# Kernel optimization log

Hardware: AMD Instinct MI355X
Metric: run time of the kernel (lower is better)

Reference implementation:

```python
import jax, jax.numpy as jnp
import numpy as np
from jax import lax

CONTEXT = 7
EPS = 1e-5  # BatchNorm2d default eps
DN = ('NCHW', 'OIHW', 'NCHW')


def _cbr(x, W, b, g, be, m, v, padding):
    # conv2d + BatchNorm (eval, running stats) + ReLU
    y = lax.conv_general_dilated(x, W, (1, 1), padding, dimension_numbers=DN)
    y = y + b[None, :, None, None]
    y = (y - m[None, :, None, None]) * (g / jnp.sqrt(v + EPS))[None, :, None, None] + be[None, :, None, None]
    return jax.nn.relu(y)


def _pool21(x):  # MaxPool2d(kernel_size=(2,1))
    return lax.reduce_window(x, -jnp.inf, lax.max, (1, 1, 2, 1), (1, 1, 2, 1), 'VALID')


def setup_inputs() -> dict:
    key = jax.random.key(0)
    ks = jax.random.split(key, 16)
    B, T, F, NC = 16, 108, 144, 25
    d = {}
    d['x'] = jax.random.normal(ks[0], (B, T, F), jnp.float32)
    d['labels'] = jax.random.randint(ks[1], (B, T), 0, NC)
    shapes = [(32, 1, 3, 3), (32, 32, 3, 3), (32, 32, 3, 3), (32, 32, 3, 3),
              (64, 32, 3, 3), (64, 64, 3, 3), (128, 64, 12, 9)]
    for i, s in enumerate(shapes, 1):
        fan_in = s[1] * s[2] * s[3]
        d[f'W{i}'] = jax.random.normal(ks[1 + i], s, jnp.float32) / np.sqrt(fan_in).astype(np.float32)
        c = s[0]
        d[f'b{i}'] = jnp.zeros((c,), jnp.float32)
        d[f'g{i}'] = jnp.ones((c,), jnp.float32)
        d[f'be{i}'] = jnp.zeros((c,), jnp.float32)
        d[f'm{i}'] = jnp.zeros((c,), jnp.float32)
        d[f'v{i}'] = jnp.ones((c,), jnp.float32)
    d['W8'] = jax.random.normal(ks[9], (NC, 128, 1, 1), jnp.float32) / np.float32(np.sqrt(128.0))
    d['b8'] = jnp.zeros((NC,), jnp.float32)
    return d


def reference(x, labels,
              W1, b1, g1, be1, m1, v1,
              W2, b2, g2, be2, m2, v2,
              W3, b3, g3, be3, m3, v3,
              W4, b4, g4, be4, m4, v4,
              W5, b5, g5, be5, m5, v5,
              W6, b6, g6, be6, m6, v6,
              W7, b7, g7, be7, m7, v7,
              W8, b8):
    B, T, F = x.shape
    win_len = 2 * CONTEXT + 1
    # permute to [B, F, T], zero-pad time by CONTEXT on both sides
    xp = jnp.pad(jnp.transpose(x, (0, 2, 1)), ((0, 0), (0, 0), (CONTEXT, CONTEXT)))
    # vectorized sliding windows (replaces the nested python loop of slices+cat)
    idx = jnp.arange(T)[:, None] + jnp.arange(win_len)[None, :]  # [T, 15]
    win = xp[:, :, idx]                                          # [B, F, T, 15]
    h = jnp.transpose(win, (0, 2, 1, 3)).reshape(B * T, 1, F, win_len)
    h = _cbr(h, W1, b1, g1, be1, m1, v1, 'SAME')
    h = _cbr(h, W2, b2, g2, be2, m2, v2, 'SAME')
    h = _cbr(h, W3, b3, g3, be3, m3, v3, 'SAME')
    h = _cbr(h, W4, b4, g4, be4, m4, v4, 'SAME')
    h = _pool21(h)  # dropout2d is identity in eval
    h = _cbr(h, W5, b5, g5, be5, m5, v5, 'VALID')
    h = _cbr(h, W6, b6, g6, be6, m6, v6, 'VALID')
    h = _pool21(h)
    h = _cbr(h, W7, b7, g7, be7, m7, v7, 'VALID')
    h = lax.conv_general_dilated(h, W8, (1, 1), 'VALID', dimension_numbers=DN) + b8[None, :, None, None]
    logits = jnp.mean(h, axis=(2, 3))  # AvgPool2d over full spatial extent
    return logits.reshape(B, T, -1)    # probs_out=True -> CRF input
```

## Files before the change

kernel.cpp:

```cpp
#include <hip/hip_runtime.h>
#include <hip/hip_bf16.h>
#include <hip/hip_fp16.h>

#define TA 71680
#define TB 69120
#define SLOT 140800
#define C6N 26112

typedef _Float16 v8h __attribute__((ext_vector_type(8)));
typedef float v4f __attribute__((ext_vector_type(4)));
typedef unsigned short u16x8 __attribute__((ext_vector_type(8)));

__device__ inline float h2f(unsigned short u) {
    union { unsigned short s; _Float16 h; } v; v.s = u; return (float)v.h;
}
__device__ inline unsigned short f2h(float f) {
    union { unsigned short s; _Float16 h; } v; v.h = (_Float16)f; return v.s;
}

__global__ void repack_k(const float* __restrict__ W, const float* __restrict__ bb,
                         const float* __restrict__ gg, const float* __restrict__ be,
                         const float* __restrict__ mm, const float* __restrict__ vv,
                         float* __restrict__ wOut, float* __restrict__ tOut,
                         int CIN, int KHW, int COUT)
{
    int gid = blockIdx.x * 256 + threadIdx.x;
    if (gid < COUT) {
        float s = gg[gid] * rsqrtf(vv[gid] + 1e-5f);
        tOut[gid] = (bb[gid] - mm[gid]) * s + be[gid];
    }
    int tot = CIN * KHW * COUT;
    if (gid >= tot) return;
    int co = gid % COUT;
    int rest = gid / COUT;
    int k = rest % KHW;
    int ci = rest / KHW;
    float s = gg[co] * rsqrtf(vv[co] + 1e-5f);
    wOut[gid] = W[(co * CIN + ci) * KHW + k] * s;
}

__global__ void repack_mfma_k(const float* __restrict__ W, const float* __restrict__ bb,
                              const float* __restrict__ gg, const float* __restrict__ be,
                              const float* __restrict__ mm, const float* __restrict__ vv,
                              unsigned short* __restrict__ frag, float* __restrict__ tOut,
                              int CIN, int NT, int HALVES)
{
    int gid = blockIdx.x * 256 + threadIdx.x;
    int COUT = NT * 16;
    if (gid < COUT) {
        float s = gg[gid] * rsqrtf(vv[gid] + 1e-5f);
        tOut[gid] = (bb[gid] - mm[gid]) * s + be[gid];
    }
    int tot = 9 * HALVES * NT * 512;
    if (gid >= tot) return;
    int j    = gid & 7;
    int lane = (gid >> 3) & 63;
    int nt   = (gid >> 9) % NT;
    int rest = (gid >> 9) / NT;
    int half = rest % HALVES;
    int khw  = rest / HALVES;
    int ci   = half * 32 + (lane >> 4) * 8 + j;
    int co   = nt * 16 + (lane & 15);
    int kh   = khw / 3, kw = khw % 3;
    float s = gg[co] * rsqrtf(vv[co] + 1e-5f);
    frag[gid] = f2h(W[((co * CIN + ci) * 3 + kh) * 3 + kw] * s);
}

__global__ void repack7_k(const float* __restrict__ W, const float* __restrict__ bb,
                          const float* __restrict__ gg, const float* __restrict__ be,
                          const float* __restrict__ mm, const float* __restrict__ vv,
                          unsigned short* __restrict__ frag, float* __restrict__ tOut)
{
    int gid = blockIdx.x * 256 + threadIdx.x;
    if (gid < 128) {
        float s = gg[gid] * rsqrtf(vv[gid] + 1e-5f);
        tOut[gid] = (bb[gid] - mm[gid]) * s + be[gid];
    }
    if (gid >= 884736) return;
    int j    = gid & 7;
    int lane = (gid >> 3) & 63;
    int nt   = (gid >> 9) & 7;
    int half = (gid >> 12) & 1;
    int khw  = gid >> 13;
    int co   = nt * 16 + (lane & 15);
    int ci   = half * 32 + (lane >> 4) * 8 + j;
    int kh   = khw / 9, kw = khw - kh * 9;
    float s = gg[co] * rsqrtf(vv[co] + 1e-5f);
    frag[gid] = f2h(W[((co * 64 + ci) * 12 + kh) * 9 + kw] * s);
}

__global__ __launch_bounds__(256) void conv1_k(
    const float* __restrict__ x, unsigned short* __restrict__ out,
    const float* __restrict__ wr, const float* __restrict__ tv,
    int c0, int cn)
{
    int gid = blockIdx.x * 256 + threadIdx.x;
    if (gid >= cn * 2160) return;
    int nl = gid / 2160, p = gid - nl * 2160;
    int f = p / 15, w = p - f * 15;
    int n = c0 + nl;
    int b = n / 108, t = n - b * 108;

    float acc[32];
#pragma unroll
    for (int i = 0; i < 32; ++i) acc[i] = 0.f;

    for (int kh = 0; kh < 3; ++kh) {
        int ff = f + kh - 1;
        if (ff < 0 || ff >= 144) continue;
        for (int kw = 0; kw < 3; ++kw) {
            int c = w + kw - 1;
            if (c < 0 || c >= 15) continue;
            int tt = t + c - 7;
            if (tt < 0 || tt >= 108) continue;
            float xval = x[(b * 108 + tt) * 144 + ff];
            const float* wp = wr + (kh * 3 + kw) * 32;
#pragma unroll
            for (int q = 0; q < 8; ++q) {
                float4 wv = *(const float4*)(wp + q * 4);
                acc[q * 4 + 0] = fmaf(xval, wv.x, acc[q * 4 + 0]);
                acc[q * 4 + 1] = fmaf(xval, wv.y, acc[q * 4 + 1]);
                acc[q * 4 + 2] = fmaf(xval, wv.z, acc[q * 4 + 2]);
                acc[q * 4 + 3] = fmaf(xval, wv.w, acc[q * 4 + 3]);
            }
        }
    }
    unsigned short* ob = out + (size_t)nl * SLOT + (f * 15 + w) * 8;
#pragma unroll
    for (int cg = 0; cg < 4; ++cg) {
        u16x8 pk;
#pragma unroll
        for (int c = 0; c < 8; ++c)
            pk[c] = f2h(fmaxf(acc[cg * 8 + c] + tv[cg * 8 + c], 0.f));
        *(u16x8*)(ob + cg * 17280) = pk;
    }
}

template<bool POOL>
__global__ __launch_bounds__(256) void conv234m_k(
    const unsigned short* __restrict__ in, unsigned short* __restrict__ out,
    const unsigned short* __restrict__ frag, const float* __restrict__ tv)
{
    __shared__ __align__(16) unsigned short sA[9824];
    const int band = blockIdx.x;
    const int n = blockIdx.y;
    const int tid = threadIdx.x;
    const int wave = tid >> 6, lane = tid & 63;
    const int m = lane & 15, quad = lane >> 4;

    {
        const float4* src = (const float4*)(in + (size_t)n * SLOT);
        float4* dst = (float4*)sA;
        for (int i = tid; i < 1224; i += 256) {
            int q = i / 306, pos = i - q * 306;
            int r = pos / 17, c = pos - r * 17;
            int ir = band * 16 + r - 1;
            int ic = c - 1;
            float4 v = {0.f, 0.f, 0.f, 0.f};
            if (ir >= 0 && ir < 144 && ic >= 0 && ic < 15)
                v = src[q * 2160 + ir * 15 + ic];
            dst[q * 307 + pos] = v;
        }
    }
    __syncthreads();

    int mt[4], la0[4];
#pragma unroll
    for (int wt = 0; wt < 4; ++wt) {
        int t = wave * 4 + wt; if (t > 14) t = 14;
        mt[wt] = t;
        int p = band * 240 + t * 16 + m;
        int r, w;
        if (POOL) { int pr = p / 30, rem = p - pr * 30; w = rem >> 1; r = pr * 2 + (rem & 1); }
        else      { r = p / 15; w = p - r * 15; }
        la0[wt] = ((r - band * 16) * 17 + w) * 8;
    }

    v4f acc[2][4];
#pragma unroll
    for (int nt = 0; nt < 2; ++nt)
#pragma unroll
        for (int wt = 0; wt < 4; ++wt) acc[nt][wt] = (v4f){0.f,0.f,0.f,0.f};

    const unsigned short* sQ = sA + quad * 307 * 8;
#pragma unroll
    for (int khw = 0; khw < 9; ++khw) {
        const int shift = ((khw / 3) * 17 + (khw % 3)) * 8;
        v8h a[4];
#pragma unroll
        for (int wt = 0; wt < 4; ++wt)
            a[wt] = *(const v8h*)(sQ + la0[wt] + shift);
#pragma unroll
        for (int nt = 0; nt < 2; ++nt) {
            v8h b = *(const v8h*)(frag + (khw * 2 + nt) * 512 + lane * 8);
#pragma unroll
            for (int wt = 0; wt < 4; ++wt)
                acc[nt][wt] = __builtin_amdgcn_mfma_f32_16x16x32_f16(a[wt], b, acc[nt][wt], 0, 0, 0);
        }
    }

    unsigned short* outN = out + (size_t)n * SLOT;
#pragma unroll
    for (int wt = 0; wt < 4; ++wt) {
        const int pb = band * 240 + mt[wt] * 16 + quad * 4;
#pragma unroll
        for (int nt = 0; nt < 2; ++nt) {
            const int co = nt * 16 + m;
            const float tb = tv[co];
            unsigned short* ob = outN + (co >> 3) * (POOL ? 9216 : 17280) + (co & 7);
            if (POOL) {
#pragma unroll
                for (int pi = 0; pi < 2; ++pi) {
                    int pe = pb + pi * 2;
                    int pr = pe / 30, rem = pe - pr * 30, w = rem >> 1;
                    float v0 = fmaxf(acc[nt][wt][pi * 2] + tb, 0.f);
                    float v1 = fmaxf(acc[nt][wt][pi * 2 + 1] + tb, 0.f);
                    ob[(pr * 16 + w) * 8] = f2h(fmaxf(v0, v1));
                }
            } else {
#pragma unroll
                for (int reg = 0; reg < 4; ++reg) {
                    int pr = pb + reg;
                    int f = pr / 15, w = pr - f * 15;
                    ob[(f * 15 + w) * 8] = f2h(fmaxf(acc[nt][wt][reg] + tb, 0.f));
                }
            }
        }
    }
}

__global__ __launch_bounds__(256) void conv5m_k(
    const unsigned short* __restrict__ in, unsigned short* __restrict__ out,
    const unsigned short* __restrict__ frag, const float* __restrict__ tv)
{
    const int n = blockIdx.y;
    const int tid = threadIdx.x;
    const int wave = tid >> 6, lane = tid & 63;
    const int m = lane & 15, quad = lane >> 4;
    const unsigned short* inN = in + (size_t)n * SLOT + quad * 9216;

    int mt[2], a0[2];
#pragma unroll
    for (int wt = 0; wt < 2; ++wt) {
        int t = blockIdx.x * 8 + wave * 2 + wt; if (t > 56) t = 56;
        mt[wt] = t;
        int p = t * 16 + m; if (p > 909) p = 909;
        int r = p / 13, w = p - r * 13;
        a0[wt] = (r * 16 + w) * 8;
    }

    v4f acc[4][2];
#pragma unroll
    for (int nt = 0; nt < 4; ++nt)
#pragma unroll
        for (int wt = 0; wt < 2; ++wt) acc[nt][wt] = (v4f){0.f,0.f,0.f,0.f};

#pragma unroll
    for (int khw = 0; khw < 9; ++khw) {
        const int shift = ((khw / 3) * 16 + (khw % 3)) * 8;
        v8h a[2];
#pragma unroll
        for (int wt = 0; wt < 2; ++wt)
            a[wt] = *(const v8h*)(inN + a0[wt] + shift);
#pragma unroll
        for (int nt = 0; nt < 4; ++nt) {
            v8h b = *(const v8h*)(frag + (khw * 4 + nt) * 512 + lane * 8);
#pragma unroll
            for (int wt = 0; wt < 2; ++wt)
                acc[nt][wt] = __builtin_amdgcn_mfma_f32_16x16x32_f16(a[wt], b, acc[nt][wt], 0, 0, 0);
        }
    }

    unsigned short* outN = out + (size_t)n * SLOT;
#pragma unroll
    for (int wt = 0; wt < 2; ++wt) {
        const int pb = mt[wt] * 16 + quad * 4;
#pragma unroll
        for (int nt = 0; nt < 4; ++nt) {
            const int co = nt * 16 + m;
            const float tb = tv[co];
            unsigned short* ob = outN + (co >> 3) * 8960 + (co & 7);
#pragma unroll
            for (int reg = 0; reg < 4; ++reg) {
                int p = pb + reg;
                if (p < 910) {
                    int r = p / 13, w = p - r * 13;
                    ob[(r * 16 + w) * 8] = f2h(fmaxf(acc[nt][wt][reg] + tb, 0.f));
                }
            }
        }
    }
}

__global__ __launch_bounds__(256) void conv6m_k(
    const unsigned short* __restrict__ in, unsigned short* __restrict__ c6,
    const unsigned short* __restrict__ frag, const float* __restrict__ tv)
{
    const int n = blockIdx.y;
    const int tid = threadIdx.x;
    const int wave = tid >> 6, lane = tid & 63;
    const int m = lane & 15, quad = lane >> 4;
    const unsigned short* inN = in + (size_t)n * SLOT;

    int mt[2], a0[2];
#pragma unroll
    for (int wt = 0; wt < 2; ++wt) {
        int t = blockIdx.x * 8 + wave * 2 + wt; if (t > 46) t = 46;
        mt[wt] = t;
        int p = t * 16 + m; if (p > 747) p = 747;
        int pr = p / 22, rem = p - pr * 22;
        int w = rem >> 1, r = pr * 2 + (rem & 1);
        a0[wt] = (r * 16 + w) * 8;
    }

    v4f acc[4][2];
#pragma unroll
    for (int nt = 0; nt < 4; ++nt)
#pragma unroll
        for (int wt = 0; wt < 2; ++wt) acc[nt][wt] = (v4f){0.f,0.f,0.f,0.f};

#pragma unroll
    for (int khw = 0; khw < 9; ++khw) {
        const int shift = ((khw / 3) * 16 + (khw % 3)) * 8;
#pragma unroll
        for (int half = 0; half < 2; ++half) {
            const unsigned short* ip = inN + (half * 4 + quad) * 8960 + shift;
            v8h a[2];
#pragma unroll
            for (int wt = 0; wt < 2; ++wt)
                a[wt] = *(const v8h*)(ip + a0[wt]);
#pragma unroll
            for (int nt = 0; nt < 4; ++nt) {
                v8h b = *(const v8h*)(frag + ((khw * 2 + half) * 4 + nt) * 512 + lane * 8);
#pragma unroll
                for (int wt = 0; wt < 2; ++wt)
                    acc[nt][wt] = __builtin_amdgcn_mfma_f32_16x16x32_f16(a[wt], b, acc[nt][wt], 0, 0, 0);
            }
        }
    }

    unsigned short* outN = c6 + (size_t)n * C6N;
#pragma unroll
    for (int wt = 0; wt < 2; ++wt) {
        const int pb = mt[wt] * 16 + quad * 4;
#pragma unroll
        for (int nt = 0; nt < 4; ++nt) {
            const int co = nt * 16 + m;
            const float tb = tv[co];
            unsigned short* ob = outN + (co >> 3) * 3264 + (co & 7);
#pragma unroll
            for (int pi = 0; pi < 2; ++pi) {
                int pe = pb + pi * 2;
                if (pe < 748) {
                    int pr = pe / 22, rem = pe - pr * 22, w = rem >> 1;
                    float v0 = fmaxf(acc[nt][wt][pi * 2] + tb, 0.f);
                    float v1 = fmaxf(acc[nt][wt][pi * 2 + 1] + tb, 0.f);
                    ob[(pr * 12 + w) * 8] = f2h(fmaxf(v0, v1));
                }
            }
        }
    }
}

__global__ __launch_bounds__(256) void conv7mfma_k(
    const unsigned short* __restrict__ c6, float* __restrict__ pooled,
    const unsigned short* __restrict__ frag7, const float* __restrict__ tv)
{
    __shared__ __align__(16) unsigned short sA[14176];
    const int n = blockIdx.x;
    const int tid = threadIdx.x;
    const int wave = tid >> 6;
    const int lane = tid & 63;
    const int m = lane & 15;
    const int quad = lane >> 4;

    int pm[5];
#pragma unroll
    for (int mt = 0; mt < 5; ++mt) {
        int p = mt * 16 + m;
        if (p >= 69) p = 0;
        pm[mt] = (p / 3) * 13 + (p % 3);
    }

    v4f acc[2][5];
#pragma unroll
    for (int t = 0; t < 2; ++t)
#pragma unroll
        for (int mt = 0; mt < 5; ++mt)
            acc[t][mt] = (v4f){0.f, 0.f, 0.f, 0.f};

    for (int half = 0; half < 2; ++half) {
        __syncthreads();
        {
            const float4* src = (const float4*)(c6 + (size_t)n * C6N + half * 13056);
            float4* dst = (float4*)sA;
            for (int i = tid; i < 1632; i += 256) {
                int q = i / 408, pos = i - q * 408;
                int h = pos / 12, w = pos - h * 12;
                dst[q * 443 + h * 13 + w] = src[i];
            }
        }
        __syncthreads();
        for (int khw = 0; khw < 108; ++khw) {
            const int off = (khw / 9) * 13 + (khw % 9);
            v8h a[5];
#pragma unroll
            for (int mt = 0; mt < 5; ++mt)
                a[mt] = *(const v8h*)(sA + (quad * 443 + pm[mt] + off) * 8);
            const unsigned short* bp = frag7
                + ((size_t)(khw * 2 + half) * 8) * 512 + lane * 8;
#pragma unroll
            for (int t = 0; t < 2; ++t) {
                const int nt = wave + t * 4;
                v8h b = *(const v8h*)(bp + nt * 512);
#pragma unroll
                for (int mt = 0; mt < 5; ++mt)
                    acc[t][mt] = __builtin_amdgcn_mfma_f32_16x16x32_f16(
                        a[mt], b, acc[t][mt], 0, 0, 0);
            }
        }
    }

    float s[2] = {0.f, 0.f};
#pragma unroll
    for (int t = 0; t < 2; ++t) {
        const float tb = tv[(wave + t * 4) * 16 + m];
#pragma unroll
        for (int mt = 0; mt < 5; ++mt) {
#pragma unroll
            for (int rr = 0; rr < 4; ++rr) {
                int p = mt * 16 + quad * 4 + rr;
                if (p < 69) s[t] += fmaxf(acc[t][mt][rr] + tb, 0.f);
            }
        }
    }
#pragma unroll
    for (int t = 0; t < 2; ++t) {
        s[t] += __shfl_xor(s[t], 16);
        s[t] += __shfl_xor(s[t], 32);
    }
    if (lane < 16) {
#pragma unroll
        for (int t = 0; t < 2; ++t)
            pooled[(size_t)n * 128 + (wave + t * 4) * 16 + lane] = s[t] * (1.f / 69.f);
    }
}

__global__ void logits_k(const float* __restrict__ pooled, const float* __restrict__ W8,
                         const float* __restrict__ b8, float* __restrict__ outg,
                         int total)
{
    int gid = blockIdx.x * 256 + threadIdx.x;
    if (gid >= total * 25) return;
    int nl = gid / 25, c = gid - nl * 25;
    const float* pp = pooled + (size_t)nl * 128;
    const float* wp = W8 + c * 128;
    float s = b8[c];
#pragma unroll
    for (int ci = 0; ci < 128; ci += 4) {
        float4 wv = *(const float4*)(wp + ci);
        float4 pv = *(const float4*)(pp + ci);
        s = fmaf(wv.x, pv.x, s);
        s = fmaf(wv.y, pv.y, s);
        s = fmaf(wv.z, pv.z, s);
        s = fmaf(wv.w, pv.w, s);
    }
    outg[(size_t)nl * 25 + c] = s;
}

extern "C" void kernel_launch(void* const* d_in, const int* in_sizes, int n_in,
                              void* d_out, int out_size, void* d_ws, size_t ws_size,
                              hipStream_t stream)
{
    const float* x = (const float*)d_in[0];
    const float* Wl[8]; const float* bl[8]; const float* gl[8];
    const float* bel[8]; const float* ml[8]; const float* vl[8];
    for (int i = 1; i <= 7; ++i) {
        int o = 2 + (i - 1) * 6;
        Wl[i]  = (const float*)d_in[o + 0];
        bl[i]  = (const float*)d_in[o + 1];
        gl[i]  = (const float*)d_in[o + 2];
        bel[i] = (const float*)d_in[o + 3];
        ml[i]  = (const float*)d_in[o + 4];
        vl[i]  = (const float*)d_in[o + 5];
    }
    const float* W8 = (const float*)d_in[44];
    const float* b8 = (const float*)d_in[45];
    float* ws = (float*)d_ws;

    float* wr1 = ws + 0;        float* t1 = ws + 288;
    unsigned short* f2b = (unsigned short*)(ws + 320);
    float* t2 = ws + 4928;
    unsigned short* f3b = (unsigned short*)(ws + 4960);
    float* t3 = ws + 9568;
    unsigned short* f4b = (unsigned short*)(ws + 9600);
    float* t4 = ws + 14208;
    unsigned short* f5b = (unsigned short*)(ws + 14240);
    float* t5 = ws + 23456;
    unsigned short* f6b = (unsigned short*)(ws + 23520);
    float* t6 = ws + 41952;
    unsigned short* f7b = (unsigned short*)(ws + 42016);
    float* t7 = ws + 484384;
    const size_t WFL = 484512;

    unsigned short* c6buf = (unsigned short*)(ws + WFL);
    const size_t C6FL = (size_t)1728 * C6N / 2;
    float* pooled = ws + WFL + C6FL;
    const size_t FIXED = WFL + C6FL + (size_t)1728 * 128;

    size_t avail_fl = ws_size / 4;
    size_t buf_halves = (avail_fl > FIXED) ? (avail_fl - FIXED) * 2 : 0;
    int Cs = (int)(buf_halves / (size_t)SLOT);
    if (Cs < 1) Cs = 1;
    if (Cs > 1728) Cs = 1728;
    unsigned short* bufA = (unsigned short*)(ws + FIXED);
    unsigned short* bufB = bufA + TA;

    auto g1 = [](int t) { return (t + 255) / 256; };

    repack_k<<<g1(288), 256, 0, stream>>>(Wl[1], bl[1], gl[1], bel[1], ml[1], vl[1], wr1, t1, 1, 9, 32);
    repack_mfma_k<<<g1(9216),  256, 0, stream>>>(Wl[2], bl[2], gl[2], bel[2], ml[2], vl[2], f2b, t2, 32, 2, 1);
    repack_mfma_k<<<g1(9216),  256, 0, stream>>>(Wl[3], bl[3], gl[3], bel[3], ml[3], vl[3], f3b, t3, 32, 2, 1);
    repack_mfma_k<<<g1(9216),  256, 0, stream>>>(Wl[4], bl[4], gl[4], bel[4], ml[4], vl[4], f4b, t4, 32, 2, 1);
    repack_mfma_k<<<g1(18432), 256, 0, stream>>>(Wl[5], bl[5], gl[5], bel[5], ml[5], vl[5], f5b, t5, 32, 4, 1);
    repack_mfma_k<<<g1(36864), 256, 0, stream>>>(Wl[6], bl[6], gl[6], bel[6], ml[6], vl[6], f6b, t6, 64, 4, 2);
    repack7_k<<<g1(884736), 256, 0, stream>>>(Wl[7], bl[7], gl[7], bel[7], ml[7], vl[7], f7b, t7);

    for (int c0 = 0; c0 < 1728; c0 += Cs) {
        int cn = (1728 - c0 < Cs) ? (1728 - c0) : Cs;
        conv1_k<<<g1(cn * 2160), 256, 0, stream>>>(x, bufA, wr1, t1, c0, cn);
        conv234m_k<false><<<dim3(9, cn), 256, 0, stream>>>(bufA, bufB, f2b, t2);
        conv234m_k<false><<<dim3(9, cn), 256, 0, stream>>>(bufB, bufA, f3b, t3);
        conv234m_k<true ><<<dim3(9, cn), 256, 0, stream>>>(bufA, bufB, f4b, t4);
        conv5m_k<<<dim3(8, cn), 256, 0, stream>>>(bufB, bufA, f5b, t5);
        conv6m_k<<<dim3(6, cn), 256, 0, stream>>>(bufA, c6buf + (size_t)c0 * C6N, f6b, t6);
    }

    conv7mfma_k<<<1728, 256, 0, stream>>>(c6buf, pooled, f7b, t7);
    logits_k<<<g1(1728 * 25), 256, 0, stream>>>(pooled, W8, b8, (float*)d_out, 1728);
}
```

Measured before the change: 1.170 ms.

## Fuse conv2/conv3/conv4 into one kernel with halo recompute in LDS

Replaces three separate conv234 launches with one kernel. Each block loads a 16-row band plus a 3-row halo, computes conv2 and conv3 over the enlarged tile in shared memory, then conv4 with fused pooling writes to global. This removes two global round trips of intermediate activations and two launches, at the cost of recomputing halo rows and using more LDS per block. It also compacts the c6 buffer layout (row stride 12 to 11) so conv7 can load with a plain linear copy, and shrinks SLOT/C6N.

New measurement: 1.134 ms. 1.03x faster.

```diff
diff --git a/kernel.cpp b/kernel.cpp
--- a/kernel.cpp
+++ b/kernel.cpp
@@ -3,9 +3,8 @@
 #include <hip/hip_fp16.h>
 
 #define TA 71680
-#define TB 69120
-#define SLOT 140800
-#define C6N 26112
+#define SLOT 108544
+#define C6N 23936
 
 typedef _Float16 v8h __attribute__((ext_vector_type(8)));
 typedef float v4f __attribute__((ext_vector_type(4)));
@@ -136,12 +135,13 @@
     }
 }
 
-template<bool POOL>
-__global__ __launch_bounds__(256) void conv234m_k(
+__global__ __launch_bounds__(256) void conv234f_k(
     const unsigned short* __restrict__ in, unsigned short* __restrict__ out,
-    const unsigned short* __restrict__ frag, const float* __restrict__ tv)
-{
-    __shared__ __align__(16) unsigned short sA[9824];
+    const unsigned short* __restrict__ f2, const unsigned short* __restrict__ f3,
+    const unsigned short* __restrict__ f4, const float* __restrict__ t2,
+    const float* __restrict__ t3, const float* __restrict__ t4)
+{
+    __shared__ __align__(16) unsigned short sm[22912];
     const int band = blockIdx.x;
     const int n = blockIdx.y;
     const int tid = threadIdx.x;
@@ -150,80 +150,178 @@
 
     {
         const float4* src = (const float4*)(in + (size_t)n * SLOT);
-        float4* dst = (float4*)sA;
-        for (int i = tid; i < 1224; i += 256) {
-            int q = i / 306, pos = i - q * 306;
-            int r = pos / 17, c = pos - r * 17;
-            int ir = band * 16 + r - 1;
-            int ic = c - 1;
-            float4 v = {0.f, 0.f, 0.f, 0.f};
-            if (ir >= 0 && ir < 144 && ic >= 0 && ic < 15)
-                v = src[q * 2160 + ir * 15 + ic];
-            dst[q * 307 + pos] = v;
+        float4* dst = (float4*)sm;
+        const float4 z = {0.f, 0.f, 0.f, 0.f};
+        for (int i = tid; i < 1656; i += 256) {
+            if (i < 1496) {
+                int q = i / 374, pos = i - q * 374;
+                int r = pos / 17, c = pos - r * 17;
+                int gr = band * 16 + r - 3;
+                int gc = c - 1;
+                float4 v = z;
+                if (gr >= 0 && gr < 144 && gc >= 0 && gc < 15)
+                    v = src[q * 2160 + gr * 15 + gc];
+                dst[q * 375 + pos + (r > 0 ? r : 0) * 0 + r * 0 + 0 + (pos - pos)] = v;
+                dst[q * 375 + pos] = v;
+            } else {
+                int j = i - 1496;
+                int q = j / 40, jj = j - q * 40;
+                int rr = jj >> 1, c2 = (jj & 1) * 16;
+                dst[1500 + q * 341 + rr * 17 + c2] = z;
+            }
         }
     }
     __syncthreads();
 
-    int mt[4], la0[4];
+    v4f acc[2][5];
+    int mt[5], la[5];
+
+#pragma unroll
+    for (int wt = 0; wt < 5; ++wt) {
+        int t = wave * 5 + wt; if (t > 18) t = 18;
+        mt[wt] = t;
+        int p = t * 16 + m; if (p >= 300) p = 299;
+        int r = p / 15, c = p - r * 15;
+        la[wt] = r * 17 + c;
+    }
+#pragma unroll
+    for (int nt = 0; nt < 2; ++nt)
+#pragma unroll
+        for (int wt = 0; wt < 5; ++wt) acc[nt][wt] = (v4f){0.f,0.f,0.f,0.f};
+#pragma unroll
+    for (int khw = 0; khw < 9; ++khw) {
+        const int sh = (khw / 3) * 17 + (khw % 3);
+        v8h a[5];
+#pragma unroll
+        for (int wt = 0; wt < 5; ++wt)
+            a[wt] = *(const v8h*)(sm + quad * 3000 + (la[wt] + sh) * 8);
+#pragma unroll
+        for (int nt = 0; nt < 2; ++nt) {
+            v8h b = *(const v8h*)(f2 + (khw * 2 + nt) * 512 + lane * 8);
+#pragma unroll
+            for (int wt = 0; wt < 5; ++wt)
+                acc[nt][wt] = __builtin_amdgcn_mfma_f32_16x16x32_f16(a[wt], b, acc[nt][wt], 0, 0, 0);
+        }
+    }
+#pragma unroll
+    for (int wt = 0; wt < 5; ++wt) {
+        const int pb = mt[wt] * 16 + quad * 4;
+#pragma unroll
+        for (int nt = 0; nt < 2; ++nt) {
+            const int co = nt * 16 + m;
+            const float tb = t2[co];
+            unsigned short* ob = sm + 12000 + (co >> 3) * 2728 + (co & 7);
+#pragma unroll
+            for (int reg = 0; reg < 4; ++reg) {
+                int p = pb + reg;
+                if (p < 300) {
+                    int r = p / 15, c = p - r * 15;
+                    ob[(r * 17 + c + 1) * 8] = f2h(fmaxf(acc[nt][wt][reg] + tb, 0.f));
+                }
+            }
+        }
+    }
+    __syncthreads();
+
+    if (tid < 144) {
+        int q = tid / 36, jj = tid - q * 36;
+        int rr = jj >> 1, c2 = (jj & 1) * 16;
+        *(float4*)((float4*)sm + q * 307 + rr * 17 + c2) = (float4){0.f,0.f,0.f,0.f};
+    }
+
+#pragma unroll
+    for (int wt = 0; wt < 5; ++wt) {
+        int t = wave * 5 + wt; if (t > 16) t = 16;
+        mt[wt] = t;
+        int p = t * 16 + m; if (p >= 270) p = 269;
+        int r = p / 15, c = p - r * 15;
+        la[wt] = r * 17 + c;
+    }
+#pragma unroll
+    for (int nt = 0; nt < 2; ++nt)
+#pragma unroll
+        for (int wt = 0; wt < 5; ++wt) acc[nt][wt] = (v4f){0.f,0.f,0.f,0.f};
+#pragma unroll
+    for (int khw = 0; khw < 9; ++khw) {
+        const int sh = (khw / 3) * 17 + (khw % 3);
+        v8h a[5];
+#pragma unroll
+        for (int wt = 0; wt < 5; ++wt)
+            a[wt] = *(const v8h*)(sm + 12000 + quad * 2728 + (la[wt] + sh) * 8);
+#pragma unroll
+        for (int nt = 0; nt < 2; ++nt) {
+            v8h b = *(const v8h*)(f3 + (khw * 2 + nt) * 512 + lane * 8);
+#pragma unroll
+            for (int wt = 0; wt < 5; ++wt)
+                acc[nt][wt] = __builtin_amdgcn_mfma_f32_16x16x32_f16(a[wt], b, acc[nt][wt], 0, 0, 0);
+        }
+    }
+#pragma unroll
+    for (int wt = 0; wt < 5; ++wt) {
+        const int pb = mt[wt] * 16 + quad * 4;
+#pragma unroll
+        for (int nt = 0; nt < 2; ++nt) {
+            const int co = nt * 16 + m;
+            const float tb = t3[co];
+            unsigned short* ob = sm + (co >> 3) * 2456 + (co & 7);
+#pragma unroll
+            for (int reg = 0; reg < 4; ++reg) {
+                int p = pb + reg;
+                if (p < 270) {
+                    int r = p / 15, c = p - r * 15;
+                    ob[(r * 17 + c + 1) * 8] = f2h(fmaxf(acc[nt][wt][reg] + tb, 0.f));
+                }
+            }
+        }
+    }
+    __syncthreads();
+
+    int mt4[4], la4[4];
 #pragma unroll
     for (int wt = 0; wt < 4; ++wt) {
         int t = wave * 4 + wt; if (t > 14) t = 14;
-        mt[wt] = t;
-        int p = band * 240 + t * 16 + m;
-        int r, w;
-        if (POOL) { int pr = p / 30, rem = p - pr * 30; w = rem >> 1; r = pr * 2 + (rem & 1); }
-        else      { r = p / 15; w = p - r * 15; }
-        la0[wt] = ((r - band * 16) * 17 + w) * 8;
-    }
-
-    v4f acc[2][4];
+        mt4[wt] = t;
+        int p = t * 16 + m;
+        int pr = p / 30, rem = p - pr * 30;
+        int w = rem >> 1, r4 = pr * 2 + (rem & 1);
+        la4[wt] = r4 * 17 + w;
+    }
+    v4f acc4[2][4];
 #pragma unroll
     for (int nt = 0; nt < 2; ++nt)
 #pragma unroll
-        for (int wt = 0; wt < 4; ++wt) acc[nt][wt] = (v4f){0.f,0.f,0.f,0.f};
-
-    const unsigned short* sQ = sA + quad * 307 * 8;
+        for (int wt = 0; wt < 4; ++wt) acc4[nt][wt] = (v4f){0.f,0.f,0.f,0.f};
 #pragma unroll
     for (int khw = 0; khw < 9; ++khw) {
-        const int shift = ((khw / 3) * 17 + (khw % 3)) * 8;
+        const int sh = (khw / 3) * 17 + (khw % 3);
         v8h a[4];
 #pragma unroll
         for (int wt = 0; wt < 4; ++wt)
-            a[wt] = *(const v8h*)(sQ + la0[wt] + shift);
+            a[wt] = *(const v8h*)(sm + quad * 2456 + (la4[wt] + sh) * 8);
 #pragma unroll
         for (int nt = 0; nt < 2; ++nt) {
-            v8h b = *(const v8h*)(frag + (khw * 2 + nt) * 512 + lane * 8);
+            v8h b = *(const v8h*)(f4 + (khw * 2 + nt) * 512 + lane * 8);
 #pragma unroll
             for (int wt = 0; wt < 4; ++wt)
-                acc[nt][wt] = __builtin_amdgcn_mfma_f32_16x16x32_f16(a[wt], b, acc[nt][wt], 0, 0, 0);
-        }
-    }
-
+                acc4[nt][wt] = __builtin_amdgcn_mfma_f32_16x16x32_f16(a[wt], b, acc4[nt][wt], 0, 0, 0);
+        }
+    }
     unsigned short* outN = out + (size_t)n * SLOT;
 #pragma unroll
     for (int wt = 0; wt < 4; ++wt) {
-        const int pb = band * 240 + mt[wt] * 16 + quad * 4;
+        const int pb = band * 240 + mt4[wt] * 16 + quad * 4;
 #pragma unroll
         for (int nt = 0; nt < 2; ++nt) {
             const int co = nt * 16 + m;
-            const float tb = tv[co];
-            unsigned short* ob = outN + (co >> 3) * (POOL ? 9216 : 17280) + (co & 7);
-            if (POOL) {
-#pragma unroll
-                for (int pi = 0; pi < 2; ++pi) {
-                    int pe = pb + pi * 2;
-                    int pr = pe / 30, rem = pe - pr * 30, w = rem >> 1;
-                    float v0 = fmaxf(acc[nt][wt][pi * 2] + tb, 0.f);
-                    float v1 = fmaxf(acc[nt][wt][pi * 2 + 1] + tb, 0.f);
-                    ob[(pr * 16 + w) * 8] = f2h(fmaxf(v0, v1));
-                }
-            } else {
-#pragma unroll
-                for (int reg = 0; reg < 4; ++reg) {
-                    int pr = pb + reg;
-                    int f = pr / 15, w = pr - f * 15;
-                    ob[(f * 15 + w) * 8] = f2h(fmaxf(acc[nt][wt][reg] + tb, 0.f));
-                }
+            const float tb = t4[co];
+            unsigned short* ob = outN + (co >> 3) * 9216 + (co & 7);
+#pragma unroll
+            for (int pi = 0; pi < 2; ++pi) {
+                int pe = pb + pi * 2;
+                int pr = pe / 30, rem = pe - pr * 30, w = rem >> 1;
+                float v0 = fmaxf(acc4[nt][wt][pi * 2] + tb, 0.f);
+                float v1 = fmaxf(acc4[nt][wt][pi * 2 + 1] + tb, 0.f);
+                ob[(pr * 16 + w) * 8] = f2h(fmaxf(v0, v1));
             }
         }
     }
@@ -347,7 +445,7 @@
         for (int nt = 0; nt < 4; ++nt) {
             const int co = nt * 16 + m;
             const float tb = tv[co];
-            unsigned short* ob = outN + (co >> 3) * 3264 + (co & 7);
+            unsigned short* ob = outN + (co >> 3) * 2992 + (co & 7);
 #pragma unroll
             for (int pi = 0; pi < 2; ++pi) {
                 int pe = pb + pi * 2;
@@ -355,7 +453,7 @@
                     int pr = pe / 22, rem = pe - pr * 22, w = rem >> 1;
                     float v0 = fmaxf(acc[nt][wt][pi * 2] + tb, 0.f);
                     float v1 = fmaxf(acc[nt][wt][pi * 2 + 1] + tb, 0.f);
-                    ob[(pr * 12 + w) * 8] = f2h(fmaxf(v0, v1));
+                    ob[(pr * 11 + w) * 8] = f2h(fmaxf(v0, v1));
                 }
             }
         }
@@ -366,7 +464,7 @@
     const unsigned short* __restrict__ c6, float* __restrict__ pooled,
     const unsigned short* __restrict__ frag7, const float* __restrict__ tv)
 {
-    __shared__ __align__(16) unsigned short sA[14176];
+    __shared__ __align__(16) unsigned short sA[11968];
     const int n = blockIdx.x;
     const int tid = threadIdx.x;
     const int wave = tid >> 6;
@@ -379,7 +477,7 @@
     for (int mt = 0; mt < 5; ++mt) {
         int p = mt * 16 + m;
         if (p >= 69) p = 0;
-        pm[mt] = (p / 3) * 13 + (p % 3);
+        pm[mt] = (p / 3) * 11 + (p % 3);
     }
 
     v4f acc[2][5];
@@ -392,21 +490,17 @@
     for (int half = 0; half < 2; ++half) {
         __syncthreads();
         {
-            const float4* src = (const float4*)(c6 + (size_t)n * C6N + half * 13056);
+            const float4* src = (const float4*)(c6 + (size_t)n * C6N + half * 11968);
             float4* dst = (float4*)sA;
-            for (int i = tid; i < 1632; i += 256) {
-                int q = i / 408, pos = i - q * 408;
-                int h = pos / 12, w = pos - h * 12;
-                dst[q * 443 + h * 13 + w] = src[i];
-            }
+            for (int i = tid; i < 1496; i += 256) dst[i] = src[i];
         }
         __syncthreads();
         for (int khw = 0; khw < 108; ++khw) {
-            const int off = (khw / 9) * 13 + (khw % 9);
+            const int off = (khw / 9) * 11 + (khw % 9);
             v8h a[5];
 #pragma unroll
             for (int mt = 0; mt < 5; ++mt)
-                a[mt] = *(const v8h*)(sA + (quad * 443 + pm[mt] + off) * 8);
+                a[mt] = *(const v8h*)(sA + quad * 2992 + (pm[mt] + off) * 8);
             const unsigned short* bp = frag7
                 + ((size_t)(khw * 2 + half) * 8) * 512 + lane * 8;
 #pragma unroll
@@ -529,9 +623,7 @@
     for (int c0 = 0; c0 < 1728; c0 += Cs) {
         int cn = (1728 - c0 < Cs) ? (1728 - c0) : Cs;
         conv1_k<<<g1(cn * 2160), 256, 0, stream>>>(x, bufA, wr1, t1, c0, cn);
-        conv234m_k<false><<<dim3(9, cn), 256, 0, stream>>>(bufA, bufB, f2b, t2);
-        conv234m_k<false><<<dim3(9, cn), 256, 0, stream>>>(bufB, bufA, f3b, t3);
-        conv234m_k<true ><<<dim3(9, cn), 256, 0, stream>>>(bufA, bufB, f4b, t4);
+        conv234f_k<<<dim3(9, cn), 256, 0, stream>>>(bufA, bufB, f2b, f3b, f4b, t2, t3, t4);
         conv5m_k<<<dim3(8, cn), 256, 0, stream>>>(bufB, bufA, f5b, t5);
         conv6m_k<<<dim3(6, cn), 256, 0, stream>>>(bufA, c6buf + (size_t)c0 * C6N, f6b, t6);
     }
```
